# Optimization experiments

Hardware: AMD Instinct MI355X
Metric: run time of the kernel (lower is better)

## Reference

```python
import jax, jax.numpy as jnp
import numpy as np

CIN, COUT, KH, KW = 128, 256, 3, 3

def setup_inputs() -> dict:
    key = jax.random.key(0)
    kx, kw = jax.random.split(key)
    x = jax.random.normal(kx, (32, CIN, 56, 56), dtype=jnp.float32)
    # kaiming normal, fan_in mode, relu gain: std = sqrt(2 / fan_in)
    fan_in = CIN * KH * KW
    weight = jax.random.normal(kw, (COUT, CIN, KH, KW), dtype=jnp.float32) * jnp.sqrt(2.0 / fan_in)
    bias = jnp.zeros((COUT,), dtype=jnp.float32)
    return {"x": x, "weight": weight, "bias": bias}

def reference(x, weight, bias):
    # VALID 2D cross-correlation (matches torch conv semantics of the manual loop)
    y = jax.lax.conv_general_dilated(
        x, weight,
        window_strides=(1, 1),
        padding="VALID",
        dimension_numbers=("NCHW", "OIHW", "NCHW"),
    )
    return y + bias[None, :, None, None]
```

## Files before the change

### kernel.cpp

```cpp
#include <hip/hip_runtime.h>
#include <hip/hip_bf16.h>

#define CIN 128
#define COUT 256
#define H 56
#define W 56
#define OH 54
#define OW 54

typedef __attribute__((ext_vector_type(8))) short short8;
typedef __attribute__((ext_vector_type(4))) float floatx4;

typedef __attribute__((address_space(3))) unsigned int  lds_u32;
typedef const __attribute__((address_space(1))) unsigned int glb_u32;

static __device__ __forceinline__ unsigned short f2bf(float f) {
  unsigned int u = __builtin_bit_cast(unsigned int, f);
  u += 0x7fffu + ((u >> 16) & 1u);
  return (unsigned short)(u >> 16);
}

__global__ void repack_w(const float* __restrict__ w, unsigned short* __restrict__ w2) {
  int idx = blockIdx.x * 256 + threadIdx.x;
  if (idx >= COUT * CIN * 9) return;
  int kw = idx % 3, t1 = idx / 3;
  int kh = t1 % 3, t2 = t1 / 3;
  int ci = t2 % CIN;
  int co = t2 / CIN;
  int c8 = ci >> 3, j = ci & 7;
  w2[((((kh * 3 + kw) * 16 + c8) * COUT + co) * 8) + j] = f2bf(w[idx]);
}

__global__ __launch_bounds__(256) void repack_x(const float* __restrict__ x,
                                                unsigned short* __restrict__ xb) {
  __shared__ float xt[56][129];
  const int h = blockIdx.x;
  const int n = blockIdx.y;
  const float* src = x + (size_t)n * CIN * (H * W) + h * W;
  #pragma unroll
  for (int r = 0; r < 28; ++r) {
    int idx = r * 256 + threadIdx.x;
    int ci = idx / 56, iw = idx % 56;
    xt[iw][ci] = src[ci * (H * W) + iw];
  }
  __syncthreads();
  unsigned short* dst = xb + ((size_t)n * H + h) * 896 * 8;
  #pragma unroll
  for (int r = 0; r < 4; ++r) {
    int g = r * 256 + threadIdx.x;
    if (g < 896) {
      int iw = g >> 4, c16 = g & 15;
      short8 v;
      #pragma unroll
      for (int j = 0; j < 8; ++j)
        v[j] = (short)f2bf(xt[iw][c16 * 8 + j]);
      int gp = iw * 16 + (c16 ^ (iw & 7));
      *reinterpret_cast<short8*>(&dst[gp * 8]) = v;
    }
  }
}

__global__ __launch_bounds__(256, 2) void conv9(
    const unsigned short* __restrict__ xb, const unsigned short* __restrict__ w2,
    const float* __restrict__ bias, float* __restrict__ out) {
  __shared__ alignas(16) unsigned short xs[3744 * 8];

  const int f = blockIdx.x;
  const int swz = (f & 7) * 108 + (f >> 3);
  const int ohp = swz % 27;
  const int n   = swz / 27;
  const int oh0 = ohp * 2;
  const int tid = threadIdx.x;
  const int wid  = tid >> 6;
  const int lane = tid & 63;

  {
    const unsigned short* src = xb + ((size_t)n * H + oh0) * 896 * 8;
    #pragma unroll
    for (int i = 0; i < 14; ++i) {
      int idx = (wid * 14 + i) * 64;
      __builtin_amdgcn_global_load_lds(
          (glb_u32*)(src + (size_t)(idx + lane) * 8),
          (lds_u32*)(&xs[idx * 8]), 16, 0, 0);
    }
  }
  asm volatile("s_waitcnt vmcnt(0)" ::: "memory");
  __syncthreads();

  const int l16  = lane & 15;
  const int cig  = lane >> 4;
  const int co_base = wid * 64;
  const int rowd = cig * 4;

  int rp[7], owp[7];
  #pragma unroll
  for (int fr = 0; fr < 7; ++fr) {
    int p = fr * 16 + l16;
    rp[fr]  = (p < 54) ? 0 : 1;
    owp[fr] = p - rp[fr] * 54;
  }

  floatx4 acc[4][7];
  #pragma unroll
  for (int m = 0; m < 4; ++m)
    #pragma unroll
    for (int fr = 0; fr < 7; ++fr)
      acc[m][fr] = (floatx4){0.f, 0.f, 0.f, 0.f};

  short8 areg[3][4];

#define AISSUE(s, slot)                                                          \
  {                                                                              \
    const int kh_ = (s) / 12, ch_ = ((s) / 3) & 3, kw_ = (s) % 3;                \
    const unsigned short* wp_ =                                                  \
        w2 + ((size_t)(((kh_ * 3 + kw_) * 16 + (ch_ * 4 + cig)) * COUT + co_base + l16)) * 8; \
    asm volatile("global_load_dwordx4 %0, %1, off"            : "=v"(areg[slot][0]) : "v"(wp_)); \
    asm volatile("global_load_dwordx4 %0, %1, off offset:256" : "=v"(areg[slot][1]) : "v"(wp_)); \
    asm volatile("global_load_dwordx4 %0, %1, off offset:512" : "=v"(areg[slot][2]) : "v"(wp_)); \
    asm volatile("global_load_dwordx4 %0, %1, off offset:768" : "=v"(areg[slot][3]) : "v"(wp_)); \
  }

  AISSUE(0, 0);
  AISSUE(1, 1);

  #pragma unroll
  for (int s = 0; s < 36; ++s) {
    if (s + 2 < 36) AISSUE(s + 2, (s + 2) % 3);

    const int kh = s / 12, ch = (s / 3) & 3, kw = s % 3;
    const int chb = ch * 4 + cig;
    short8 b[7];
    #pragma unroll
    for (int fr = 0; fr < 7; ++fr) {
      const int iwl = owp[fr] + kw;
      const int c16x = chb ^ (iwl & 7);
      const int boff = ((rp[fr] + kh) * 896 + iwl * 16 + c16x) * 8;
      b[fr] = *reinterpret_cast<const short8*>(&xs[boff]);
    }

    if (s < 34)       asm volatile("s_waitcnt vmcnt(8)" ::: "memory");
    else if (s == 34) asm volatile("s_waitcnt vmcnt(4)" ::: "memory");
    else              asm volatile("s_waitcnt vmcnt(0)" ::: "memory");
    __builtin_amdgcn_sched_barrier(0);

    __builtin_amdgcn_s_setprio(1);
    #pragma unroll
    for (int m = 0; m < 4; ++m)
      #pragma unroll
      for (int fr = 0; fr < 7; ++fr)
        acc[m][fr] = __builtin_amdgcn_mfma_f32_16x16x32_bf16(
            areg[s % 3][m], b[fr], acc[m][fr], 0, 0, 0);
    __builtin_amdgcn_s_setprio(0);
  }
#undef AISSUE

  #pragma unroll
  for (int m = 0; m < 4; ++m) {
    #pragma unroll
    for (int reg = 0; reg < 4; ++reg) {
      int co = co_base + m * 16 + rowd + reg;
      float bvv = bias[co];
      float* opb = out + (((size_t)n * COUT + co) * OH + oh0) * OW;
      #pragma unroll
      for (int fr = 0; fr < 7; ++fr) {
        int p = fr * 16 + l16;
        if (p < 108)
          opb[rp[fr] * OW + owp[fr]] = acc[m][fr][reg] + bvv;
      }
    }
  }
}

#define CSTR 136
#define IWP 66

__global__ __launch_bounds__(512, 4) void conv_fb(
    const float* __restrict__ x, const unsigned short* __restrict__ w2,
    const float* __restrict__ bias, float* __restrict__ out) {
  __shared__ alignas(16) unsigned short xsf[4 * IWP * CSTR];

  const int ohp = blockIdx.x;
  const int n   = blockIdx.y;
  const int oh0 = ohp * 2;
  const int tid = threadIdx.x;

  {
    short8 zz = {0, 0, 0, 0, 0, 0, 0, 0};
    for (int i = tid; i < 4 * 10 * 17; i += 512) {
      int r = i / 170, rem = i % 170;
      int iw = 56 + rem / 17, g = rem % 17;
      *reinterpret_cast<short8*>(&xsf[(r * IWP + iw) * CSTR + g * 8]) = zz;
    }
  }
  for (int s = tid; s < 3584; s += 512) {
    int iw = s % 56;
    int t  = s / 56;
    int c8 = t & 15, r = t >> 4;
    const float* xp = x + (size_t)n * CIN * (H * W) + (oh0 + r) * W + iw;
    short8 v;
    #pragma unroll
    for (int j = 0; j < 8; ++j)
      v[j] = (short)f2bf(xp[(size_t)(c8 * 8 + j) * (H * W)]);
    *reinterpret_cast<short8*>(&xsf[(r * IWP + iw) * CSTR + c8 * 8]) = v;
  }
  __syncthreads();

  const int wid  = tid >> 6;
  const int lane = tid & 63;
  const int wm   = wid >> 1;
  const int wn   = wid & 1;
  const int l16  = lane & 15;
  const int cig  = lane >> 4;

  const int co_base = wm * 64;
  const int oh = oh0 + wn;

  floatx4 acc[4][4];
  #pragma unroll
  for (int m = 0; m < 4; ++m)
    #pragma unroll
    for (int nr = 0; nr < 4; ++nr)
      acc[m][nr] = (floatx4){0.f, 0.f, 0.f, 0.f};

  for (int kh = 0; kh < 3; ++kh) {
    const int row = wn + kh;
    #pragma unroll
    for (int ch = 0; ch < 4; ++ch) {
      const int bbase = (row * IWP + l16) * CSTR + ch * 32 + cig * 8;
      #pragma unroll
      for (int kw = 0; kw < 3; ++kw) {
        const unsigned short* wp =
            w2 + ((size_t)(((kh * 3 + kw) * 16 + (ch * 4 + cig)) * COUT + co_base + l16)) * 8;
        short8 a[4];
        #pragma unroll
        for (int m = 0; m < 4; ++m)
          a[m] = *reinterpret_cast<const short8*>(wp + m * 16 * 8);
        short8 b[4];
        #pragma unroll
        for (int nr = 0; nr < 4; ++nr)
          b[nr] = *reinterpret_cast<const short8*>(&xsf[bbase + (nr * 16 + kw) * CSTR]);
        #pragma unroll
        for (int m = 0; m < 4; ++m)
          #pragma unroll
          for (int nr = 0; nr < 4; ++nr)
            acc[m][nr] = __builtin_amdgcn_mfma_f32_16x16x32_bf16(a[m], b[nr], acc[m][nr], 0, 0, 0);
      }
    }
  }

  const int rowd = cig * 4;
  #pragma unroll
  for (int m = 0; m < 4; ++m) {
    #pragma unroll
    for (int reg = 0; reg < 4; ++reg) {
      int co = co_base + m * 16 + rowd + reg;
      float bvv = bias[co];
      float* op = out + (((size_t)n * COUT + co) * OH + oh) * OW;
      #pragma unroll
      for (int nr = 0; nr < 4; ++nr) {
        int ow = nr * 16 + l16;
        if (ow < OW) op[ow] = acc[m][nr][reg] + bvv;
      }
    }
  }
}

extern "C" void kernel_launch(void* const* d_in, const int* in_sizes, int n_in,
                              void* d_out, int out_size, void* d_ws, size_t ws_size,
                              hipStream_t stream) {
  (void)in_sizes; (void)n_in; (void)out_size;
  const float* x    = (const float*)d_in[0];
  const float* w    = (const float*)d_in[1];
  const float* bias = (const float*)d_in[2];
  float* out = (float*)d_out;

  const size_t W2_BYTES = (size_t)9 * 16 * COUT * 8 * 2;
  const size_t XB_BYTES = (size_t)32 * H * 896 * 8 * 2;
  unsigned short* w2 = (unsigned short*)d_ws;

  repack_w<<<dim3((COUT * CIN * 9 + 255) / 256), dim3(256), 0, stream>>>(w, w2);

  if (ws_size >= W2_BYTES + XB_BYTES) {
    unsigned short* xb = (unsigned short*)((char*)d_ws + W2_BYTES);
    repack_x<<<dim3(56, 32), dim3(256), 0, stream>>>(x, xb);
    conv9<<<dim3(864), dim3(256), 0, stream>>>(xb, w2, bias, out);
  } else {
    conv_fb<<<dim3(27, 32), dim3(512), 0, stream>>>(x, w2, bias, out);
  }
}
```

Baseline: 84.66 us.

## Enlarge conv tile to four output rows with 512-thread blocks

The conv kernel now processes four output rows per block with eight waves, split as four output-channel groups by two row pairs. Each block loads six input rows into LDS instead of four, so less input is re-read per output row. Each weight fragment loaded is reused only within its wave. Weight prefetch depth drops from two stages ahead to one, and the first weight load now overlaps the LDS fill. An unused fallback weight repack kernel is also added. The grid shrinks from 864 to 448 blocks, which may hurt load balance across CUs, and the shallower weight prefetch may expose more load latency.

```diff
diff --git a/kernel.cpp b/kernel.cpp
--- a/kernel.cpp
+++ b/kernel.cpp
@@ -60,37 +60,42 @@
   }
 }
 
-__global__ __launch_bounds__(256, 2) void conv9(
+__global__ __launch_bounds__(512, 2) void conv10(
     const unsigned short* __restrict__ xb, const unsigned short* __restrict__ w2,
     const float* __restrict__ bias, float* __restrict__ out) {
-  __shared__ alignas(16) unsigned short xs[3744 * 8];
+  __shared__ alignas(16) unsigned short xs[5440 * 8];
 
   const int f = blockIdx.x;
-  const int swz = (f & 7) * 108 + (f >> 3);
-  const int ohp = swz % 27;
-  const int n   = swz / 27;
-  const int oh0 = ohp * 2;
+  const int swz = (f & 7) * 56 + (f >> 3);
+  const int ohq = swz % 14;
+  const int n   = swz / 14;
+  const int oh0 = ohq * 4;
   const int tid = threadIdx.x;
   const int wid  = tid >> 6;
   const int lane = tid & 63;
 
   {
-    const unsigned short* src = xb + ((size_t)n * H + oh0) * 896 * 8;
-    #pragma unroll
-    for (int i = 0; i < 14; ++i) {
-      int idx = (wid * 14 + i) * 64;
-      __builtin_amdgcn_global_load_lds(
-          (glb_u32*)(src + (size_t)(idx + lane) * 8),
-          (lds_u32*)(&xs[idx * 8]), 16, 0, 0);
-    }
-  }
-  asm volatile("s_waitcnt vmcnt(0)" ::: "memory");
-  __syncthreads();
-
+    #pragma unroll
+    for (int i = 0; i < 11; ++i) {
+      int c = i * 8 + wid;
+      if (c < 84) {
+        int row = c / 14, part = c % 14;
+        int srow = oh0 + row; if (srow > 55) srow = 55;
+        const unsigned short* src =
+            xb + (((size_t)n * H + srow) * 896 + part * 64 + lane) * 8;
+        __builtin_amdgcn_global_load_lds(
+            (glb_u32*)src, (lds_u32*)(&xs[(size_t)c * 64 * 8]), 16, 0, 0);
+      }
+    }
+  }
+
+  const int wm   = wid & 3;
+  const int wn   = wid >> 2;
   const int l16  = lane & 15;
   const int cig  = lane >> 4;
-  const int co_base = wid * 64;
+  const int co_base = wm * 64;
   const int rowd = cig * 4;
+  const int rbase = 2 * wn;
 
   int rp[7], owp[7];
   #pragma unroll
@@ -100,14 +105,7 @@
     owp[fr] = p - rp[fr] * 54;
   }
 
-  floatx4 acc[4][7];
-  #pragma unroll
-  for (int m = 0; m < 4; ++m)
-    #pragma unroll
-    for (int fr = 0; fr < 7; ++fr)
-      acc[m][fr] = (floatx4){0.f, 0.f, 0.f, 0.f};
-
-  short8 areg[3][4];
+  short8 areg[2][4];
 
 #define AISSUE(s, slot)                                                          \
   {                                                                              \
@@ -121,11 +119,19 @@
   }
 
   AISSUE(0, 0);
-  AISSUE(1, 1);
+  asm volatile("s_waitcnt vmcnt(0)" ::: "memory");
+  __syncthreads();
+
+  floatx4 acc[4][7];
+  #pragma unroll
+  for (int m = 0; m < 4; ++m)
+    #pragma unroll
+    for (int fr = 0; fr < 7; ++fr)
+      acc[m][fr] = (floatx4){0.f, 0.f, 0.f, 0.f};
 
   #pragma unroll
   for (int s = 0; s < 36; ++s) {
-    if (s + 2 < 36) AISSUE(s + 2, (s + 2) % 3);
+    if (s < 35) AISSUE(s + 1, (s + 1) & 1);
 
     const int kh = s / 12, ch = (s / 3) & 3, kw = s % 3;
     const int chb = ch * 4 + cig;
@@ -134,13 +140,12 @@
     for (int fr = 0; fr < 7; ++fr) {
       const int iwl = owp[fr] + kw;
       const int c16x = chb ^ (iwl & 7);
-      const int boff = ((rp[fr] + kh) * 896 + iwl * 16 + c16x) * 8;
+      const int boff = ((rbase + rp[fr] + kh) * 896 + iwl * 16 + c16x) * 8;
       b[fr] = *reinterpret_cast<const short8*>(&xs[boff]);
     }
 
-    if (s < 34)       asm volatile("s_waitcnt vmcnt(8)" ::: "memory");
-    else if (s == 34) asm volatile("s_waitcnt vmcnt(4)" ::: "memory");
-    else              asm volatile("s_waitcnt vmcnt(0)" ::: "memory");
+    if (s < 35) asm volatile("s_waitcnt vmcnt(4)" ::: "memory");
+    else        asm volatile("s_waitcnt vmcnt(0)" ::: "memory");
     __builtin_amdgcn_sched_barrier(0);
 
     __builtin_amdgcn_s_setprio(1);
@@ -149,7 +154,7 @@
       #pragma unroll
       for (int fr = 0; fr < 7; ++fr)
         acc[m][fr] = __builtin_amdgcn_mfma_f32_16x16x32_bf16(
-            areg[s % 3][m], b[fr], acc[m][fr], 0, 0, 0);
+            areg[s & 1][m], b[fr], acc[m][fr], 0, 0, 0);
     __builtin_amdgcn_s_setprio(0);
   }
 #undef AISSUE
@@ -160,12 +165,13 @@
     for (int reg = 0; reg < 4; ++reg) {
       int co = co_base + m * 16 + rowd + reg;
       float bvv = bias[co];
-      float* opb = out + (((size_t)n * COUT + co) * OH + oh0) * OW;
       #pragma unroll
       for (int fr = 0; fr < 7; ++fr) {
         int p = fr * 16 + l16;
-        if (p < 108)
-          opb[rp[fr] * OW + owp[fr]] = acc[m][fr][reg] + bvv;
+        int oh = oh0 + rbase + rp[fr];
+        if (p < 108 && oh < OH)
+          out[((((size_t)n * COUT + co) * OH + oh) * OW) + owp[fr]] =
+              acc[m][fr][reg] + bvv;
       }
     }
   }
@@ -173,6 +179,17 @@
 
 #define CSTR 136
 #define IWP 66
+
+__global__ void repack_w_fb(const float* __restrict__ w, unsigned short* __restrict__ w2) {
+  int idx = blockIdx.x * 256 + threadIdx.x;
+  if (idx >= COUT * CIN * 9) return;
+  int kw = idx % 3, t1 = idx / 3;
+  int kh = t1 % 3, t2 = t1 / 3;
+  int ci = t2 % CIN;
+  int co = t2 / CIN;
+  int c8 = ci >> 3, j = ci & 7;
+  w2[((((kh * 3 + kw) * 16 + c8) * COUT + co) * 8) + j] = f2bf(w[idx]);
+}
 
 __global__ __launch_bounds__(512, 4) void conv_fb(
     const float* __restrict__ x, const unsigned short* __restrict__ w2,
@@ -283,7 +300,7 @@
   if (ws_size >= W2_BYTES + XB_BYTES) {
     unsigned short* xb = (unsigned short*)((char*)d_ws + W2_BYTES);
     repack_x<<<dim3(56, 32), dim3(256), 0, stream>>>(x, xb);
-    conv9<<<dim3(864), dim3(256), 0, stream>>>(xb, w2, bias, out);
+    conv10<<<dim3(448), dim3(512), 0, stream>>>(xb, w2, bias, out);
   } else {
     conv_fb<<<dim3(27, 32), dim3(512), 0, stream>>>(x, w2, bias, out);
   }
```

New measurement: 103.6 us. 22.4% more time.

## Fuse weight and input repacking into one launch; shrink A-prefetch to double buffer

Applied to the files above, without the earlier changes.

Merges the weight repack and input repack kernels into a single prepack launch: the extra blocks past 1792 convert weights, with 32 elements per thread. This removes one kernel launch and its gap. The conv kernel's weight-register prefetch goes from triple buffering (two stages ahead) to double buffering (one stage ahead). That frees VGPRs but leaves less time to hide global load latency. The fallback path keeps a separate weight repack kernel.

```diff
diff --git a/kernel.cpp b/kernel.cpp
--- a/kernel.cpp
+++ b/kernel.cpp
@@ -20,22 +20,28 @@
   return (unsigned short)(u >> 16);
 }
 
-__global__ void repack_w(const float* __restrict__ w, unsigned short* __restrict__ w2) {
-  int idx = blockIdx.x * 256 + threadIdx.x;
-  if (idx >= COUT * CIN * 9) return;
-  int kw = idx % 3, t1 = idx / 3;
-  int kh = t1 % 3, t2 = t1 / 3;
-  int ci = t2 % CIN;
-  int co = t2 / CIN;
-  int c8 = ci >> 3, j = ci & 7;
-  w2[((((kh * 3 + kw) * 16 + c8) * COUT + co) * 8) + j] = f2bf(w[idx]);
-}
-
-__global__ __launch_bounds__(256) void repack_x(const float* __restrict__ x,
-                                                unsigned short* __restrict__ xb) {
+__global__ __launch_bounds__(256) void prepack(const float* __restrict__ x,
+                                               unsigned short* __restrict__ xb,
+                                               const float* __restrict__ w,
+                                               unsigned short* __restrict__ w2) {
+  if (blockIdx.x >= 1792) {
+    const int wb = blockIdx.x - 1792;
+    int base = wb * 8192 + threadIdx.x;
+    #pragma unroll
+    for (int k2 = 0; k2 < 32; ++k2) {
+      int idx = base + k2 * 256;
+      int kw = idx % 3, t1 = idx / 3;
+      int kh = t1 % 3, t2 = t1 / 3;
+      int ci = t2 % CIN;
+      int co = t2 / CIN;
+      int c8 = ci >> 3, j = ci & 7;
+      w2[((((kh * 3 + kw) * 16 + c8) * COUT + co) * 8) + j] = f2bf(w[idx]);
+    }
+    return;
+  }
   __shared__ float xt[56][129];
-  const int h = blockIdx.x;
-  const int n = blockIdx.y;
+  const int h = blockIdx.x % 56;
+  const int n = blockIdx.x / 56;
   const float* src = x + (size_t)n * CIN * (H * W) + h * W;
   #pragma unroll
   for (int r = 0; r < 28; ++r) {
@@ -60,7 +66,7 @@
   }
 }
 
-__global__ __launch_bounds__(256, 2) void conv9(
+__global__ __launch_bounds__(256, 2) void conv11(
     const unsigned short* __restrict__ xb, const unsigned short* __restrict__ w2,
     const float* __restrict__ bias, float* __restrict__ out) {
   __shared__ alignas(16) unsigned short xs[3744 * 8];
@@ -107,7 +113,7 @@
     for (int fr = 0; fr < 7; ++fr)
       acc[m][fr] = (floatx4){0.f, 0.f, 0.f, 0.f};
 
-  short8 areg[3][4];
+  short8 areg[2][4];
 
 #define AISSUE(s, slot)                                                          \
   {                                                                              \
@@ -121,11 +127,10 @@
   }
 
   AISSUE(0, 0);
-  AISSUE(1, 1);
 
   #pragma unroll
   for (int s = 0; s < 36; ++s) {
-    if (s + 2 < 36) AISSUE(s + 2, (s + 2) % 3);
+    if (s < 35) AISSUE(s + 1, (s + 1) & 1);
 
     const int kh = s / 12, ch = (s / 3) & 3, kw = s % 3;
     const int chb = ch * 4 + cig;
@@ -138,9 +143,8 @@
       b[fr] = *reinterpret_cast<const short8*>(&xs[boff]);
     }
 
-    if (s < 34)       asm volatile("s_waitcnt vmcnt(8)" ::: "memory");
-    else if (s == 34) asm volatile("s_waitcnt vmcnt(4)" ::: "memory");
-    else              asm volatile("s_waitcnt vmcnt(0)" ::: "memory");
+    if (s < 35) asm volatile("s_waitcnt vmcnt(4)" ::: "memory");
+    else        asm volatile("s_waitcnt vmcnt(0)" ::: "memory");
     __builtin_amdgcn_sched_barrier(0);
 
     __builtin_amdgcn_s_setprio(1);
@@ -149,7 +153,7 @@
       #pragma unroll
       for (int fr = 0; fr < 7; ++fr)
         acc[m][fr] = __builtin_amdgcn_mfma_f32_16x16x32_bf16(
-            areg[s % 3][m], b[fr], acc[m][fr], 0, 0, 0);
+            areg[s & 1][m], b[fr], acc[m][fr], 0, 0, 0);
     __builtin_amdgcn_s_setprio(0);
   }
 #undef AISSUE
@@ -173,6 +177,17 @@
 
 #define CSTR 136
 #define IWP 66
+
+__global__ void repack_w_fb(const float* __restrict__ w, unsigned short* __restrict__ w2) {
+  int idx = blockIdx.x * 256 + threadIdx.x;
+  if (idx >= COUT * CIN * 9) return;
+  int kw = idx % 3, t1 = idx / 3;
+  int kh = t1 % 3, t2 = t1 / 3;
+  int ci = t2 % CIN;
+  int co = t2 / CIN;
+  int c8 = ci >> 3, j = ci & 7;
+  w2[((((kh * 3 + kw) * 16 + c8) * COUT + co) * 8) + j] = f2bf(w[idx]);
+}
 
 __global__ __launch_bounds__(512, 4) void conv_fb(
     const float* __restrict__ x, const unsigned short* __restrict__ w2,
@@ -278,13 +293,12 @@
   const size_t XB_BYTES = (size_t)32 * H * 896 * 8 * 2;
   unsigned short* w2 = (unsigned short*)d_ws;
 
-  repack_w<<<dim3((COUT * CIN * 9 + 255) / 256), dim3(256), 0, stream>>>(w, w2);
-
   if (ws_size >= W2_BYTES + XB_BYTES) {
     unsigned short* xb = (unsigned short*)((char*)d_ws + W2_BYTES);
-    repack_x<<<dim3(56, 32), dim3(256), 0, stream>>>(x, xb);
-    conv9<<<dim3(864), dim3(256), 0, stream>>>(xb, w2, bias, out);
+    prepack<<<dim3(1828), dim3(256), 0, stream>>>(x, xb, w, w2);
+    conv11<<<dim3(864), dim3(256), 0, stream>>>(xb, w2, bias, out);
   } else {
+    repack_w_fb<<<dim3((COUT * CIN * 9 + 255) / 256), dim3(256), 0, stream>>>(w, w2);
     conv_fb<<<dim3(27, 32), dim3(512), 0, stream>>>(x, w2, bias, out);
   }
 }
```

Measured after the change: 78.78 us. 7.0% less time.
